# Performance work log

Measured on AMD Instinct MI355X. Metric: run time of the kernel, lower is better.

Reference implementation:

```python
import jax, jax.numpy as jnp
import numpy as np

EMBED_DIM = 1024
NB_HEADS = 16
HEAD_DIM = EMBED_DIM // NB_HEADS


def setup_inputs() -> dict:
    key = jax.random.key(0)
    ks = jax.random.split(key, 5)
    B, N, D = 4, 2048, EMBED_DIM
    scale = 1.0 / np.sqrt(D)
    return {
        "x": jax.random.normal(ks[0], (B, N, D), dtype=jnp.float32),
        "qkv_w": jax.random.normal(ks[1], (3 * D, D), dtype=jnp.float32) * scale,
        "qkv_b": jax.random.normal(ks[2], (3 * D,), dtype=jnp.float32) * 0.02,
        "proj_w": jax.random.normal(ks[3], (D, D), dtype=jnp.float32) * scale,
        "proj_b": jax.random.normal(ks[4], (D,), dtype=jnp.float32) * 0.02,
    }


def reference(x, qkv_w, qkv_b, proj_w, proj_b):
    B, N, D = x.shape
    H, Hd = NB_HEADS, HEAD_DIM
    # qkv projection: torch Linear => x @ W.T + b
    qkv = x @ qkv_w.T + qkv_b                       # [B, N, 3D]
    qkv = qkv.reshape(B, N, 3, H, Hd)
    q = jnp.transpose(qkv[:, :, 0], (0, 2, 1, 3))   # [B, H, N, Hd]
    k = jnp.transpose(qkv[:, :, 1], (0, 2, 1, 3))
    v = jnp.transpose(qkv[:, :, 2], (0, 2, 1, 3))
    scores = jnp.einsum("bhnd,bhmd->bhnm", q, k) * (Hd ** -0.5)  # [B,H,N,N]
    attn = jax.nn.softmax(scores, axis=-1)
    out = jnp.einsum("bhnm,bhmd->bhnd", attn, v)    # [B, H, N, Hd]
    out = jnp.transpose(out, (0, 2, 1, 3)).reshape(B, N, D)
    out = out @ proj_w.T + proj_b
    return out
```

## Files before the change

### kernel.cpp

```cpp
#include <hip/hip_runtime.h>


typedef __attribute__((ext_vector_type(8))) short bf16x8;
typedef __attribute__((ext_vector_type(4))) short s16x4;
typedef __attribute__((ext_vector_type(4))) float f32x4;
typedef __attribute__((ext_vector_type(16))) float f32x16;
typedef __attribute__((ext_vector_type(4))) unsigned u32x4;

#define LOG2E 1.44269504088896340736f

__device__ static inline short f2bf(float f) {
  unsigned u = __builtin_bit_cast(unsigned, f);
  unsigned r = (u + 0x7fffu + ((u >> 16) & 1u)) >> 16;
  return (short)r;
}
__device__ static inline unsigned cvtpk_bf16(float lo, float hi) {
  unsigned r;
  asm("v_cvt_pk_bf16_f32 %0, %1, %2" : "=v"(r) : "v"(lo), "v"(hi));
  return r;
}
__device__ static inline float exp2_hw(float x) {
#if __has_builtin(__builtin_amdgcn_exp2f)
  return __builtin_amdgcn_exp2f(x);
#else
  float r;
  asm("v_exp_f32 %0, %1" : "=v"(r) : "v"(x));
  return r;
#endif
}

__device__ static inline void gload_lds16(const void* g, void* l) {
  __builtin_amdgcn_global_load_lds(
      (const __attribute__((address_space(1))) void*)g,
      (__attribute__((address_space(3))) void*)l, 16, 0, 0);
}

__global__ void cvt_f32_bf16(const float* __restrict__ in, short* __restrict__ out, int n4) {
  int i = blockIdx.x * 256 + threadIdx.x;
  if (i < n4) {
    float4 v = ((const float4*)in)[i];
    s16x4 o4 = { f2bf(v.x), f2bf(v.y), f2bf(v.z), f2bf(v.w) };
    ((s16x4*)out)[i] = o4;
  }
}

template <int EPI>
__global__ __launch_bounds__(256, 3) void gemm_bt(
    const short* __restrict__ A, const short* __restrict__ Bm,
    const float* __restrict__ bias, int K,
    short* __restrict__ qo, short* __restrict__ ko, short* __restrict__ vto,
    float* __restrict__ outf) {
  __shared__ __align__(16) char smem[32768];
  const int tid = threadIdx.x, lane = tid & 63, w = tid >> 6;
  const int wm = w >> 1, wn = w & 1;
  const int bm = blockIdx.y, bn = blockIdx.x;

  f32x4 acc[4][4];
  const f32x4 z4 = {0.f, 0.f, 0.f, 0.f};
#pragma unroll
  for (int m = 0; m < 4; ++m)
#pragma unroll
    for (int n = 0; n < 4; ++n) acc[m][n] = z4;

  const short* Abase = A + (size_t)bm * 128 * K;
  const short* Bbase = Bm + (size_t)bn * 128 * K;

  const int cl = (lane & 3) ^ ((lane >> 2) & 3) ^ (lane >> 4);
  auto STAGE = [&](int k0, int buf) {
    char* As_ = smem + buf * 16384;
    char* Bs_ = As_ + 8192;
#pragma unroll
    for (int j = 0; j < 2; ++j) {
      int ia = w * 2 + j;
      int row = ia * 16 + (lane >> 2);
      gload_lds16(Abase + (size_t)row * K + k0 + cl * 8, As_ + ia * 1024);
      gload_lds16(Bbase + (size_t)row * K + k0 + cl * 8, Bs_ + ia * 1024);
    }
  };

  STAGE(0, 0);
  __syncthreads();

  int cur = 0;
  for (int k0 = 0; k0 < K; k0 += 32) {
    if (k0 + 32 < K) STAGE(k0 + 32, cur ^ 1);

    const char* As_ = smem + cur * 16384;
    const char* Bs_ = As_ + 8192;
    bf16x8 af[4], bf[4];
#pragma unroll
    for (int m = 0; m < 4; ++m) {
      int r = wm * 64 + m * 16 + (lane & 15);
      af[m] = *(const bf16x8*)(As_ + r * 64 +
                               (((lane >> 4) ^ (r & 3) ^ ((r >> 2) & 3)) << 4));
    }
#pragma unroll
    for (int n = 0; n < 4; ++n) {
      int r = wn * 64 + n * 16 + (lane & 15);
      bf[n] = *(const bf16x8*)(Bs_ + r * 64 +
                               (((lane >> 4) ^ (r & 3) ^ ((r >> 2) & 3)) << 4));
    }
#pragma unroll
    for (int m = 0; m < 4; ++m)
#pragma unroll
      for (int n = 0; n < 4; ++n)
        acc[m][n] = __builtin_amdgcn_mfma_f32_16x16x32_bf16(af[m], bf[n], acc[m][n], 0, 0, 0);

    __syncthreads();
    cur ^= 1;
  }

  if (EPI == 0) {
    const int which = bn >> 3;
    const int hh = ((bn & 7) << 1) | wn;
    const int bidx = bm >> 4;
    const size_t bh = (size_t)bidx * 16 + hh;
#pragma unroll
    for (int nf = 0; nf < 4; ++nf) {
      int dd = nf * 16 + (lane & 15);
      float bv = bias[bn * 128 + wn * 64 + dd];
#pragma unroll
      for (int m = 0; m < 4; ++m) {
        int nr0 = (bm & 15) * 128 + wm * 64 + m * 16 + ((lane >> 4) << 2);
        if (which == 2) {
          int nper = (nr0 & ~12) | ((nr0 & 4) << 1) | ((nr0 & 8) >> 1);
          s16x4 pk;
#pragma unroll
          for (int r = 0; r < 4; ++r) pk[r] = f2bf(acc[m][nf][r] + bv);
          *(s16x4*)(vto + (bh * 64 + dd) * 2048 + nper) = pk;
        } else if (which == 0) {
          short* dst = qo + (bh * 2048 + nr0) * 64 + dd;
#pragma unroll
          for (int r = 0; r < 4; ++r)
            dst[(size_t)r * 64] = f2bf((acc[m][nf][r] + bv) * (0.125f * LOG2E));
        } else {
          short* dst = ko + (bh * 2048 + nr0) * 64 + dd;
#pragma unroll
          for (int r = 0; r < 4; ++r) dst[(size_t)r * 64] = f2bf(acc[m][nf][r] + bv);
        }
      }
    }
  } else {
#pragma unroll
    for (int nf = 0; nf < 4; ++nf) {
      int gn = bn * 128 + wn * 64 + nf * 16 + (lane & 15);
      float bv = bias[gn];
#pragma unroll
      for (int m = 0; m < 4; ++m) {
        int gm0 = bm * 128 + wm * 64 + m * 16 + ((lane >> 4) << 2);
        float* dst = outf + (size_t)gm0 * 1024 + gn;
#pragma unroll
        for (int r = 0; r < 4; ++r) dst[(size_t)r * 1024] = acc[m][nf][r] + bv;
      }
    }
  }
}

#define BUILD_PF(pf, sX0, sX1)                                                 \
  {                                                                            \
    u32x4 wd0 = {cvtpk_bf16(sX0[0], sX0[1]), cvtpk_bf16(sX0[2], sX0[3]),       \
                 cvtpk_bf16(sX0[4], sX0[5]), cvtpk_bf16(sX0[6], sX0[7])};      \
    pf[0] = __builtin_bit_cast(bf16x8, wd0);                                   \
    u32x4 wd1 = {cvtpk_bf16(sX0[8], sX0[9]), cvtpk_bf16(sX0[10], sX0[11]),     \
                 cvtpk_bf16(sX0[12], sX0[13]), cvtpk_bf16(sX0[14], sX0[15])};  \
    pf[1] = __builtin_bit_cast(bf16x8, wd1);                                   \
    u32x4 wd2 = {cvtpk_bf16(sX1[0], sX1[1]), cvtpk_bf16(sX1[2], sX1[3]),       \
                 cvtpk_bf16(sX1[4], sX1[5]), cvtpk_bf16(sX1[6], sX1[7])};      \
    pf[2] = __builtin_bit_cast(bf16x8, wd2);                                   \
    u32x4 wd3 = {cvtpk_bf16(sX1[8], sX1[9]), cvtpk_bf16(sX1[10], sX1[11]),     \
                 cvtpk_bf16(sX1[12], sX1[13]), cvtpk_bf16(sX1[14], sX1[15])};  \
    pf[3] = __builtin_bit_cast(bf16x8, wd3);                                   \
  }

__global__ __launch_bounds__(256, 2) void attn_kernel(
    const short* __restrict__ q, const short* __restrict__ kk,
    const short* __restrict__ vt, short* __restrict__ ao) {
  __shared__ __align__(16) char smem[32768];
  const int tid = threadIdx.x, lane = tid & 63, w = tid >> 6;
  const int r31 = lane & 31, h = lane >> 5;
  const int id = blockIdx.x;
  const int xcd = id & 7, p = id >> 3;
  const int bh = xcd * 8 + (p >> 3);
  const int qblk = p & 7;
  const int q0 = qblk * 256 + w * 64;

  const short* qptr = q + ((size_t)bh * 2048 + q0 + r31) * 64 + h * 8;
  const short* kgl = kk + (size_t)bh * 2048 * 64;
  const short* vgl = vt + (size_t)bh * 64 * 2048;

  const int srow = w * 16 + (lane >> 3);
  const int scol = ((lane & 7) * 8) ^ ((lane >> 3) << 3);
  const int ldst = w * 2048;

  bf16x8 qfA[4], qfB[4];
#pragma unroll
  for (int dk = 0; dk < 4; ++dk) {
    qfA[dk] = *(const bf16x8*)(qptr + dk * 16);
    qfB[dk] = *(const bf16x8*)(qptr + 32 * 64 + dk * 16);
  }

  f32x16 oA0, oA1, oB0, oB1;
#pragma unroll
  for (int e = 0; e < 16; ++e) { oA0[e] = 0.f; oA1[e] = 0.f; oB0[e] = 0.f; oB1[e] = 0.f; }
  float lsA[8], lsB[8];
#pragma unroll
  for (int e = 0; e < 8; ++e) { lsA[e] = 0.f; lsB[e] = 0.f; }

#pragma unroll
  for (int j = 0; j < 2; ++j) {
    gload_lds16(kgl + (size_t)(srow + j * 8) * 64 + scol, smem + ldst + j * 1024);
    gload_lds16(vgl + (size_t)(srow + j * 8) * 2048 + scol, smem + 8192 + ldst + j * 1024);
  }
  __syncthreads();

  int cur = 0;
  for (int t = 0; t < 2048; t += 64) {
    const char* Kb = smem + cur * 16384;
    const char* Vb = smem + cur * 16384 + 8192;

    if (t + 64 < 2048) {
      char* nb = (char*)smem + (cur ^ 1) * 16384;
#pragma unroll
      for (int j = 0; j < 2; ++j) {
        gload_lds16(kgl + (size_t)(t + 64 + srow + j * 8) * 64 + scol, nb + ldst + j * 1024);
        gload_lds16(vgl + (size_t)(srow + j * 8) * 2048 + (t + 64) + scol, nb + 8192 + ldst + j * 1024);
      }
    }

    bf16x8 kf0[4], kf1[4];
#pragma unroll
    for (int dk = 0; dk < 4; ++dk) {
      int cb = (dk * 32 + h * 16) ^ ((r31 & 7) << 4);
      kf0[dk] = *(const bf16x8*)(Kb + r31 * 128 + cb);
      kf1[dk] = *(const bf16x8*)(Kb + (32 + r31) * 128 + cb);
    }

    f32x16 sA0, sA1, sB0, sB1;
#pragma unroll
    for (int e = 0; e < 16; ++e) { sA0[e] = 0.f; sA1[e] = 0.f; sB0[e] = 0.f; sB1[e] = 0.f; }
#pragma unroll
    for (int dk = 0; dk < 4; ++dk) {
      sA0 = __builtin_amdgcn_mfma_f32_32x32x16_bf16(kf0[dk], qfA[dk], sA0, 0, 0, 0);
      sA1 = __builtin_amdgcn_mfma_f32_32x32x16_bf16(kf1[dk], qfA[dk], sA1, 0, 0, 0);
      sB0 = __builtin_amdgcn_mfma_f32_32x32x16_bf16(kf0[dk], qfB[dk], sB0, 0, 0, 0);
      sB1 = __builtin_amdgcn_mfma_f32_32x32x16_bf16(kf1[dk], qfB[dk], sB1, 0, 0, 0);
    }

    bf16x8 vf[8];
#pragma unroll
    for (int db = 0; db < 2; ++db)
#pragma unroll
      for (int ks = 0; ks < 4; ++ks) {
        int cb = (ks * 32 + h * 16) ^ ((r31 & 7) << 4);
        vf[db * 4 + ks] = *(const bf16x8*)(Vb + (db * 32 + r31) * 128 + cb);
      }

#pragma unroll
    for (int e = 0; e < 16; ++e) {
      sA0[e] = exp2_hw(sA0[e]);
      sA1[e] = exp2_hw(sA1[e]);
      sB0[e] = exp2_hw(sB0[e]);
      sB1[e] = exp2_hw(sB1[e]);
    }
#pragma unroll
    for (int e = 0; e < 8; ++e) {
      lsA[e] += (sA0[e] + sA0[e + 8]) + (sA1[e] + sA1[e + 8]);
      lsB[e] += (sB0[e] + sB0[e + 8]) + (sB1[e] + sB1[e + 8]);
    }

    bf16x8 pfA[4], pfB[4];
    BUILD_PF(pfA, sA0, sA1);
    BUILD_PF(pfB, sB0, sB1);

#pragma unroll
    for (int ks = 0; ks < 4; ++ks) {
      oA0 = __builtin_amdgcn_mfma_f32_32x32x16_bf16(vf[ks], pfA[ks], oA0, 0, 0, 0);
      oA1 = __builtin_amdgcn_mfma_f32_32x32x16_bf16(vf[4 + ks], pfA[ks], oA1, 0, 0, 0);
      oB0 = __builtin_amdgcn_mfma_f32_32x32x16_bf16(vf[ks], pfB[ks], oB0, 0, 0, 0);
      oB1 = __builtin_amdgcn_mfma_f32_32x32x16_bf16(vf[4 + ks], pfB[ks], oB1, 0, 0, 0);
    }

    __syncthreads();
    cur ^= 1;
  }

  const int b = bh >> 4, hd = bh & 15;
#pragma unroll
  for (int st = 4; st >= 1; st >>= 1)
#pragma unroll
    for (int e = 0; e < 4; ++e)
      if (e < st) { lsA[e] += lsA[e + st]; lsB[e] += lsB[e + st]; }
  float lsumA = lsA[0] + __shfl_xor(lsA[0], 32);
  float lsumB = lsB[0] + __shfl_xor(lsB[0], 32);
  float invA = 1.f / lsumA, invB = 1.f / lsumB;

  short* orowA = ao + ((size_t)b * 2048 + q0 + r31) * 1024 + hd * 64;
  short* orowB = orowA + (size_t)32 * 1024;
#pragma unroll
  for (int s2 = 0; s2 < 4; ++s2) {
    s16x4 a0, a1, b0, b1;
#pragma unroll
    for (int r = 0; r < 4; ++r) {
      a0[r] = f2bf(oA0[4 * s2 + r] * invA);
      a1[r] = f2bf(oA1[4 * s2 + r] * invA);
      b0[r] = f2bf(oB0[4 * s2 + r] * invB);
      b1[r] = f2bf(oB1[4 * s2 + r] * invB);
    }
    *(s16x4*)(orowA + 8 * s2 + 4 * h) = a0;
    *(s16x4*)(orowA + 32 + 8 * s2 + 4 * h) = a1;
    *(s16x4*)(orowB + 8 * s2 + 4 * h) = b0;
    *(s16x4*)(orowB + 32 + 8 * s2 + 4 * h) = b1;
  }
}

extern "C" void kernel_launch(void* const* d_in, const int* in_sizes, int n_in,
                              void* d_out, int out_size, void* d_ws, size_t ws_size,
                              hipStream_t stream) {
  const float* x = (const float*)d_in[0];
  const float* qkv_w = (const float*)d_in[1];
  const float* qkv_b = (const float*)d_in[2];
  const float* proj_w = (const float*)d_in[3];
  const float* proj_b = (const float*)d_in[4];
  float* out = (float*)d_out;

  char* ws = (char*)d_ws;
  short* xb    = (short*)(ws + 0);
  short* wqkv  = (short*)(ws + 16777216);
  short* wproj = (short*)(ws + 23068672);
  short* qb    = (short*)(ws + 25165824);
  short* kb    = (short*)(ws + 41943040);
  short* vtb   = (short*)(ws + 58720256);
  short* aob   = (short*)(ws + 75497472);

  cvt_f32_bf16<<<8192, 256, 0, stream>>>(x, xb, 2097152);
  cvt_f32_bf16<<<3072, 256, 0, stream>>>(qkv_w, wqkv, 786432);
  cvt_f32_bf16<<<1024, 256, 0, stream>>>(proj_w, wproj, 262144);

  gemm_bt<0><<<dim3(24, 64), 256, 0, stream>>>(xb, wqkv, qkv_b, 1024, qb, kb, vtb, nullptr);
  attn_kernel<<<512, 256, 0, stream>>>(qb, kb, vtb, aob);
  gemm_bt<1><<<dim3(8, 64), 256, 0, stream>>>(aob, wproj, proj_b, 1024, nullptr, nullptr, nullptr, out);
}
```

Baseline: 186.3 us.

## Triple-buffer GEMM LDS pipeline with explicit waitcnt and fuse weight conversions

The GEMM main loop moves from double buffering with a full __syncthreads per K step to a three-stage LDS ring. Each step issues loads two tiles ahead and waits only on the older vmcnt group before a bare s_barrier. K is fixed at 1024 so the loop can be fully unrolled. The two weight-conversion launches are merged into one kernel to save a launch. In exchange, LDS use rises to 48KB per block, which may limit the 3-blocks-per-CU occupancy target, and correctness now depends on hand-written waitcnt counts.

```diff
diff --git a/kernel.cpp b/kernel.cpp
--- a/kernel.cpp
+++ b/kernel.cpp
@@ -43,17 +43,30 @@
     ((s16x4*)out)[i] = o4;
   }
 }
+__global__ void cvt_weights(const float* __restrict__ wa, short* __restrict__ oa,
+                            const float* __restrict__ wb, short* __restrict__ ob) {
+  int i = blockIdx.x * 256 + threadIdx.x;
+  const float4* src;
+  s16x4* dst;
+  int j;
+  if (i < 786432) { src = (const float4*)wa; dst = (s16x4*)oa; j = i; }
+  else            { src = (const float4*)wb; dst = (s16x4*)ob; j = i - 786432; }
+  float4 v = src[j];
+  s16x4 o4 = { f2bf(v.x), f2bf(v.y), f2bf(v.z), f2bf(v.w) };
+  dst[j] = o4;
+}
 
 template <int EPI>
 __global__ __launch_bounds__(256, 3) void gemm_bt(
     const short* __restrict__ A, const short* __restrict__ Bm,
-    const float* __restrict__ bias, int K,
+    const float* __restrict__ bias,
     short* __restrict__ qo, short* __restrict__ ko, short* __restrict__ vto,
     float* __restrict__ outf) {
-  __shared__ __align__(16) char smem[32768];
+  __shared__ __align__(16) char smem[49152];
   const int tid = threadIdx.x, lane = tid & 63, w = tid >> 6;
   const int wm = w >> 1, wn = w & 1;
   const int bm = blockIdx.y, bn = blockIdx.x;
+  const int K = 1024;
 
   f32x4 acc[4][4];
   const f32x4 z4 = {0.f, 0.f, 0.f, 0.f};
@@ -66,9 +79,9 @@
   const short* Bbase = Bm + (size_t)bn * 128 * K;
 
   const int cl = (lane & 3) ^ ((lane >> 2) & 3) ^ (lane >> 4);
-  auto STAGE = [&](int k0, int buf) {
-    char* As_ = smem + buf * 16384;
-    char* Bs_ = As_ + 8192;
+  auto STAGE = [&](int k0, char* base) {
+    char* As_ = base;
+    char* Bs_ = base + 8192;
 #pragma unroll
     for (int j = 0; j < 2; ++j) {
       int ia = w * 2 + j;
@@ -78,15 +91,9 @@
     }
   };
 
-  STAGE(0, 0);
-  __syncthreads();
-
-  int cur = 0;
-  for (int k0 = 0; k0 < K; k0 += 32) {
-    if (k0 + 32 < K) STAGE(k0 + 32, cur ^ 1);
-
-    const char* As_ = smem + cur * 16384;
-    const char* Bs_ = As_ + 8192;
+  auto COMPUTE = [&](const char* base) {
+    const char* As_ = base;
+    const char* Bs_ = base + 8192;
     bf16x8 af[4], bf[4];
 #pragma unroll
     for (int m = 0; m < 4; ++m) {
@@ -105,10 +112,28 @@
 #pragma unroll
       for (int n = 0; n < 4; ++n)
         acc[m][n] = __builtin_amdgcn_mfma_f32_16x16x32_bf16(af[m], bf[n], acc[m][n], 0, 0, 0);
-
-    __syncthreads();
-    cur ^= 1;
-  }
+  };
+
+  STAGE(0, smem);
+  STAGE(32, smem + 16384);
+  asm volatile("s_waitcnt vmcnt(4)" ::: "memory");
+  __builtin_amdgcn_s_barrier();
+  __builtin_amdgcn_sched_barrier(0);
+
+#pragma unroll
+  for (int i = 0; i < 30; ++i) {
+    STAGE(32 * (i + 2), smem + ((i + 2) % 3) * 16384);
+    COMPUTE(smem + (i % 3) * 16384);
+    asm volatile("s_waitcnt lgkmcnt(0)" ::: "memory");
+    asm volatile("s_waitcnt vmcnt(4)" ::: "memory");
+    __builtin_amdgcn_s_barrier();
+    __builtin_amdgcn_sched_barrier(0);
+  }
+  COMPUTE(smem + (30 % 3) * 16384);
+  asm volatile("s_waitcnt lgkmcnt(0) vmcnt(0)" ::: "memory");
+  __builtin_amdgcn_s_barrier();
+  __builtin_amdgcn_sched_barrier(0);
+  COMPUTE(smem + (31 % 3) * 16384);
 
   if (EPI == 0) {
     const int which = bn >> 3;
@@ -333,10 +358,9 @@
   short* aob   = (short*)(ws + 75497472);
 
   cvt_f32_bf16<<<8192, 256, 0, stream>>>(x, xb, 2097152);
-  cvt_f32_bf16<<<3072, 256, 0, stream>>>(qkv_w, wqkv, 786432);
-  cvt_f32_bf16<<<1024, 256, 0, stream>>>(proj_w, wproj, 262144);
-
-  gemm_bt<0><<<dim3(24, 64), 256, 0, stream>>>(xb, wqkv, qkv_b, 1024, qb, kb, vtb, nullptr);
+  cvt_weights<<<4096, 256, 0, stream>>>(qkv_w, wqkv, proj_w, wproj);
+
+  gemm_bt<0><<<dim3(24, 64), 256, 0, stream>>>(xb, wqkv, qkv_b, qb, kb, vtb, nullptr);
   attn_kernel<<<512, 256, 0, stream>>>(qb, kb, vtb, aob);
-  gemm_bt<1><<<dim3(8, 64), 256, 0, stream>>>(aob, wproj, proj_b, 1024, nullptr, nullptr, nullptr, out);
-}
+  gemm_bt<1><<<dim3(8, 64), 256, 0, stream>>>(aob, wproj, proj_b, nullptr, nullptr, nullptr, out);
+}
```

Result: faster. 178.1 us, median of 2 (-4.4%).
